# Kernel tuning notes

Measured on AMD Instinct MI355X. Metric: run time of the kernel, lower is better.

## Reference

```python
import jax, jax.numpy as jnp
import numpy as np

B, DIM, N = 16, 512, 4096


def setup_inputs() -> dict:
    key = jax.random.key(0)
    kx, kq, kk, kv = jax.random.split(key, 4)
    scale = 1.0 / np.sqrt(DIM)
    return {
        "x": jax.random.normal(kx, (B, DIM, N), dtype=jnp.float32),
        "Wq": jax.random.normal(kq, (DIM, DIM), dtype=jnp.float32) * scale,
        "Wk": jax.random.normal(kk, (DIM, DIM), dtype=jnp.float32) * scale,
        "Wv": jax.random.normal(kv, (DIM, DIM), dtype=jnp.float32) * scale,
    }


def reference(x, Wq, Wk, Wv):
    # x: [B, dim, N]; 1x1 conv over channel dim == matmul with [dim_out, dim_in]
    dim = x.shape[1]
    temperature = jnp.sqrt(jnp.asarray(dim, dtype=x.dtype))
    q = jnp.einsum("dc,bcn->bdn", Wq, x)  # [B, dim, N]
    k = jnp.einsum("dc,bcn->bdn", Wk, x)
    v = jnp.einsum("dc,bcn->bdn", Wv, x)
    # channel attention: contract over N points -> [B, dim, dim]
    attn = jnp.einsum("bdn,ben->bde", q / temperature, k)
    attn = jax.nn.softmax(attn, axis=-1)
    out = jnp.einsum("bde,ben->bdn", attn, v)  # [B, dim, N]
    return out
```

## Files before the change

kernel.cpp:

```cpp
#include <hip/hip_runtime.h>
#include <hip/hip_bf16.h>
#include <math.h>

#define DIMC 512
#define NPT  4096
#define BATCH 16
#define KSPLIT 4

typedef __bf16 bf16x4 __attribute__((ext_vector_type(4)));
typedef __bf16 bf16x8 __attribute__((ext_vector_type(8)));
typedef float  f32x4  __attribute__((ext_vector_type(4)));

typedef const __attribute__((address_space(1))) unsigned int guint;
typedef __attribute__((address_space(3))) unsigned int luint;

__device__ inline void gl_lds16(const void* g, void* l) {
  __builtin_amdgcn_global_load_lds((guint*)g, (luint*)l, 16, 0, 0);
}

__device__ inline unsigned short bfbits(float f) {
  union { __bf16 h; unsigned short u; } cv;
  cv.h = (__bf16)f;
  return cv.u;
}

__global__ __launch_bounds__(256, 4) void gram_split(
    const __bf16* __restrict__ xb, float* __restrict__ Gp)
{
  static const int TI[10] = {0,0,0,0,1,1,1,2,2,3};
  static const int TJ[10] = {0,1,2,3,1,2,3,2,3,3};
  const int id = blockIdx.x;
  const int xcd = id & 7, slot = id >> 3;
  const int g = slot / 10, t = slot % 10;
  const int pair = xcd + 8 * g;
  const int b = pair >> 2, s = pair & 3;
  const int m0 = TI[t] * 128, n0 = TJ[t] * 128;

  const __bf16* A = xb + (long)b * DIMC * NPT;
  float* C = Gp + (long)pair * DIMC * DIMC;

  __shared__ alignas(16) __bf16 As[128 * 32];
  __shared__ alignas(16) __bf16 Bs[128 * 32];

  const int tid  = threadIdx.x;
  const int wave = tid >> 6, lane = tid & 63;
  const int wr = wave >> 1, wc = wave & 1;
  const int q = lane >> 4, p = lane & 15;
  const int r4 = lane >> 2;
  const int koff = (lane & 3) * 8;

  f32x4 acc[4][4];
#pragma unroll
  for (int i = 0; i < 4; ++i)
#pragma unroll
    for (int j = 0; j < 4; ++j) acc[i][j] = (f32x4){0.f, 0.f, 0.f, 0.f};

  const __bf16* gA = A + (long)m0 * NPT;
  const __bf16* gB = A + (long)n0 * NPT;
  const int kbeg = s * (NPT / KSPLIT), kend = kbeg + NPT / KSPLIT;

  for (int k0 = kbeg; k0 < kend; k0 += 32) {
    __syncthreads();
#pragma unroll
    for (int h = 0; h < 2; ++h) {
      const int chunk = wave + h * 4;
      gl_lds16(gA + (long)(chunk * 16 + r4) * NPT + k0 + koff, &As[chunk * 512]);
      gl_lds16(gB + (long)(chunk * 16 + r4) * NPT + k0 + koff, &Bs[chunk * 512]);
    }
    __syncthreads();

    bf16x8 af[4], bfv[4];
#pragma unroll
    for (int i = 0; i < 4; ++i)
      af[i] = ((const bf16x8*)As)[(wr * 64 + i * 16 + p) * 4 + q];
#pragma unroll
    for (int j = 0; j < 4; ++j)
      bfv[j] = ((const bf16x8*)Bs)[(wc * 64 + j * 16 + p) * 4 + q];
#pragma unroll
    for (int i = 0; i < 4; ++i)
#pragma unroll
      for (int j = 0; j < 4; ++j)
        acc[i][j] = __builtin_amdgcn_mfma_f32_16x16x32_bf16(af[i], bfv[j], acc[i][j], 0, 0, 0);
  }

#pragma unroll
  for (int i = 0; i < 4; ++i) {
    const int row = m0 + wr * 64 + i * 16 + q * 4;
#pragma unroll
    for (int j = 0; j < 4; ++j) {
      const int col = n0 + wc * 64 + j * 16 + p;
#pragma unroll
      for (int r = 0; r < 4; ++r)
        C[(long)(row + r) * DIMC + col] = acc[i][j][r];
    }
  }
}

__global__ __launch_bounds__(256) void gram_reduce_mirror(
    const float* __restrict__ Gp, __bf16* __restrict__ Gh, __bf16* __restrict__ Gl)
{
  const int bid = blockIdx.x;
  const int b = bid / 36;
  int rem = bid % 36, I = 0;
  while (rem >= 8 - I) { rem -= 8 - I; ++I; }
  const int J = I + rem;

  __shared__ float T[64][65];
  const int tid = threadIdx.x;
  const int r = tid >> 2, c0 = (tid & 3) * 16;

  float v[16];
#pragma unroll
  for (int e = 0; e < 16; ++e) v[e] = 0.f;
#pragma unroll
  for (int s = 0; s < KSPLIT; ++s) {
    const float* src = Gp + (long)(b * KSPLIT + s) * DIMC * DIMC
                          + (long)(I * 64 + r) * DIMC + J * 64 + c0;
#pragma unroll
    for (int q = 0; q < 4; ++q) {
      float4 t4 = ((const float4*)src)[q];
      v[q * 4 + 0] += t4.x; v[q * 4 + 1] += t4.y;
      v[q * 4 + 2] += t4.z; v[q * 4 + 3] += t4.w;
    }
  }

  const long gbase = (long)b * DIMC * DIMC;
#pragma unroll
  for (int q = 0; q < 4; ++q) {
    bf16x4 h, l;
#pragma unroll
    for (int e = 0; e < 4; ++e) {
      float f = v[q * 4 + e];
      __bf16 hh = (__bf16)f;
      h[e] = hh; l[e] = (__bf16)(f - (float)hh);
    }
    const long o = gbase + (long)(I * 64 + r) * DIMC + J * 64 + c0 + q * 4;
    *(bf16x4*)(Gh + o) = h;
    *(bf16x4*)(Gl + o) = l;
  }
#pragma unroll
  for (int e = 0; e < 16; ++e) T[r][c0 + e] = v[e];
  __syncthreads();
  if (I != J) {
#pragma unroll
    for (int q = 0; q < 4; ++q) {
      bf16x4 h, l;
#pragma unroll
      for (int e = 0; e < 4; ++e) {
        float f = T[c0 + q * 4 + e][r];
        __bf16 hh = (__bf16)f;
        h[e] = hh; l[e] = (__bf16)(f - (float)hh);
      }
      const long o = gbase + (long)(J * 64 + r) * DIMC + I * 64 + c0 + q * 4;
      *(bf16x4*)(Gh + o) = h;
      *(bf16x4*)(Gl + o) = l;
    }
  }
}

template <bool SPLIT_OUT>
__global__ __launch_bounds__(256, 4) void gemm3_nt(
    const __bf16* __restrict__ Ah, const __bf16* __restrict__ Al,
    const __bf16* __restrict__ Bh, const __bf16* __restrict__ Bl,
    float* __restrict__ Cf, __bf16* __restrict__ Ch, __bf16* __restrict__ Cl,
    int K, long sA, long sB, long sC, float alpha)
{
  const int b = blockIdx.z;
  Ah += (long)b * sA;  Al += (long)b * sA;
  Bh += (long)b * sB;  Bl += (long)b * sB;
  const int m0 = blockIdx.y * 64, n0 = blockIdx.x * 128;

  __shared__ alignas(16) __bf16 sAh[64 * 32],  sAl[64 * 32];
  __shared__ alignas(16) __bf16 sBh[128 * 32], sBl[128 * 32];

  const int tid  = threadIdx.x;
  const int wave = tid >> 6, lane = tid & 63;
  const int wr = wave >> 1, wc = wave & 1;
  const int q = lane >> 4, p = lane & 15;
  const int r4 = lane >> 2;
  const int koff = (lane & 3) * 8;

  f32x4 acc[2][4];
#pragma unroll
  for (int i = 0; i < 2; ++i)
#pragma unroll
    for (int j = 0; j < 4; ++j) acc[i][j] = (f32x4){0.f, 0.f, 0.f, 0.f};

  const long arow = (long)(m0 + wave * 16 + r4) * K + koff;

  for (int k0 = 0; k0 < K; k0 += 32) {
    __syncthreads();
    gl_lds16(Ah + arow + k0, &sAh[wave * 512]);
    gl_lds16(Al + arow + k0, &sAl[wave * 512]);
#pragma unroll
    for (int h = 0; h < 2; ++h) {
      const int chunk = wave + h * 4;
      const long brow = (long)(n0 + chunk * 16 + r4) * K + koff + k0;
      gl_lds16(Bh + brow, &sBh[chunk * 512]);
      gl_lds16(Bl + brow, &sBl[chunk * 512]);
    }
    __syncthreads();

    bf16x8 fah[2], fal[2], fbh[4], fbl[4];
#pragma unroll
    for (int i = 0; i < 2; ++i) {
      const int idx = (wr * 32 + i * 16 + p) * 4 + q;
      fah[i] = ((const bf16x8*)sAh)[idx];
      fal[i] = ((const bf16x8*)sAl)[idx];
    }
#pragma unroll
    for (int j = 0; j < 4; ++j) {
      const int idx = (wc * 64 + j * 16 + p) * 4 + q;
      fbh[j] = ((const bf16x8*)sBh)[idx];
      fbl[j] = ((const bf16x8*)sBl)[idx];
    }
#pragma unroll
    for (int i = 0; i < 2; ++i)
#pragma unroll
      for (int j = 0; j < 4; ++j) {
        acc[i][j] = __builtin_amdgcn_mfma_f32_16x16x32_bf16(fah[i], fbh[j], acc[i][j], 0, 0, 0);
        acc[i][j] = __builtin_amdgcn_mfma_f32_16x16x32_bf16(fah[i], fbl[j], acc[i][j], 0, 0, 0);
        acc[i][j] = __builtin_amdgcn_mfma_f32_16x16x32_bf16(fal[i], fbh[j], acc[i][j], 0, 0, 0);
      }
  }

#pragma unroll
  for (int i = 0; i < 2; ++i) {
    const int row = m0 + wr * 32 + i * 16 + q * 4;
#pragma unroll
    for (int j = 0; j < 4; ++j) {
      const int col = n0 + wc * 64 + j * 16 + p;
#pragma unroll
      for (int r = 0; r < 4; ++r) {
        const float f = acc[i][j][r] * alpha;
        const long o = (long)b * sC + (long)(row + r) * DIMC + col;
        if (SPLIT_OUT) {
          __bf16 hh = (__bf16)f;
          Ch[o] = hh;
          Cl[o] = (__bf16)(f - (float)hh);
        } else {
          Cf[o] = f;
        }
      }
    }
  }
}

__global__ __launch_bounds__(256, 4) void gemm_nt64x128(
    const __bf16* __restrict__ A, const __bf16* __restrict__ B,
    __bf16* __restrict__ C, int K, long sA, long sB, long sC)
{
  const int b = blockIdx.z;
  A += (long)b * sA;  B += (long)b * sB;  C += (long)b * sC;
  const int m0 = blockIdx.y * 64, n0 = blockIdx.x * 128;

  __shared__ alignas(16) __bf16 As[64 * 32];
  __shared__ alignas(16) __bf16 Bs[128 * 32];

  const int tid  = threadIdx.x;
  const int wave = tid >> 6, lane = tid & 63;
  const int wr = wave >> 1, wc = wave & 1;
  const int q = lane >> 4, p = lane & 15;
  const int r4 = lane >> 2;
  const int koff = (lane & 3) * 8;

  f32x4 acc[2][4];
#pragma unroll
  for (int i = 0; i < 2; ++i)
#pragma unroll
    for (int j = 0; j < 4; ++j) acc[i][j] = (f32x4){0.f, 0.f, 0.f, 0.f};

  const long arow = (long)(m0 + wave * 16 + r4) * K + koff;

  for (int k0 = 0; k0 < K; k0 += 32) {
    __syncthreads();
    gl_lds16(A + arow + k0, &As[wave * 512]);
#pragma unroll
    for (int h = 0; h < 2; ++h) {
      const int chunk = wave + h * 4;
      gl_lds16(B + (long)(n0 + chunk * 16 + r4) * K + koff + k0, &Bs[chunk * 512]);
    }
    __syncthreads();

    bf16x8 af[2], bfv[4];
#pragma unroll
    for (int i = 0; i < 2; ++i)
      af[i] = ((const bf16x8*)As)[(wr * 32 + i * 16 + p) * 4 + q];
#pragma unroll
    for (int j = 0; j < 4; ++j)
      bfv[j] = ((const bf16x8*)Bs)[(wc * 64 + j * 16 + p) * 4 + q];
#pragma unroll
    for (int i = 0; i < 2; ++i)
#pragma unroll
      for (int j = 0; j < 4; ++j)
        acc[i][j] = __builtin_amdgcn_mfma_f32_16x16x32_bf16(af[i], bfv[j], acc[i][j], 0, 0, 0);
  }

#pragma unroll
  for (int i = 0; i < 2; ++i) {
    const int row = m0 + wr * 32 + i * 16 + q * 4;
#pragma unroll
    for (int j = 0; j < 4; ++j) {
      const int col = n0 + wc * 64 + j * 16 + p;
#pragma unroll
      for (int r = 0; r < 4; ++r)
        C[(long)(row + r) * DIMC + col] = (__bf16)acc[i][j][r];
    }
  }
}

__global__ __launch_bounds__(256, 2) void gemm_final(
    const __bf16* __restrict__ Mm, const __bf16* __restrict__ xt,
    float* __restrict__ out)
{
  const int id = blockIdx.x;
  const int xcd = id & 7, slot = id >> 3;
  const int g = slot >> 7, tile = slot & 127;
  const int b = xcd + 8 * g;
  const int m0 = (tile >> 5) * 128, n0 = (tile & 31) * 128;

  const __bf16* A = Mm + (long)b * DIMC * DIMC;
  const __bf16* B = xt + (long)b * NPT * DIMC;
  float* C = out + (long)b * DIMC * NPT;
  const int K = DIMC;

  __shared__ alignas(16) __bf16 As[128 * 32];
  __shared__ alignas(16) __bf16 Bs[128 * 32];

  const int tid  = threadIdx.x;
  const int wave = tid >> 6, lane = tid & 63;
  const int wr = wave >> 1, wc = wave & 1;
  const int q = lane >> 4, p = lane & 15;
  const int r4 = lane >> 2;
  const int koff = (lane & 3) * 8;

  f32x4 acc[4][4];
#pragma unroll
  for (int i = 0; i < 4; ++i)
#pragma unroll
    for (int j = 0; j < 4; ++j) acc[i][j] = (f32x4){0.f, 0.f, 0.f, 0.f};

  const __bf16* gA = A + (long)m0 * K;
  const __bf16* gB = B + (long)n0 * K;

  for (int k0 = 0; k0 < K; k0 += 32) {
    __syncthreads();
#pragma unroll
    for (int h = 0; h < 2; ++h) {
      const int chunk = wave + h * 4;
      gl_lds16(gA + (long)(chunk * 16 + r4) * K + k0 + koff, &As[chunk * 512]);
      gl_lds16(gB + (long)(chunk * 16 + r4) * K + k0 + koff, &Bs[chunk * 512]);
    }
    __syncthreads();

    bf16x8 af[4], bfv[4];
#pragma unroll
    for (int i = 0; i < 4; ++i)
      af[i] = ((const bf16x8*)As)[(wr * 64 + i * 16 + p) * 4 + q];
#pragma unroll
    for (int j = 0; j < 4; ++j)
      bfv[j] = ((const bf16x8*)Bs)[(wc * 64 + j * 16 + p) * 4 + q];
#pragma unroll
    for (int i = 0; i < 4; ++i)
#pragma unroll
      for (int j = 0; j < 4; ++j)
        acc[i][j] = __builtin_amdgcn_mfma_f32_16x16x32_bf16(af[i], bfv[j], acc[i][j], 0, 0, 0);
  }

#pragma unroll
  for (int i = 0; i < 4; ++i) {
    const int row = m0 + wr * 64 + i * 16 + q * 4;
#pragma unroll
    for (int j = 0; j < 4; ++j) {
      const int col = n0 + wc * 64 + j * 16 + p;
#pragma unroll
      for (int r = 0; r < 4; ++r)
        C[(long)(row + r) * NPT + col] = acc[i][j][r];
    }
  }
}

__global__ __launch_bounds__(256) void transpose_convert_x(
    const float* __restrict__ x, __bf16* __restrict__ xt,
    __bf16* __restrict__ xb)
{
  const int b = blockIdx.z;
  const int n0 = blockIdx.x * 64, c0 = blockIdx.y * 64;
  const float* X = x + (long)b * DIMC * NPT;
  __bf16* XT = xt + (long)b * NPT * DIMC;
  __bf16* XB = xb + (long)b * DIMC * NPT;

  __shared__ unsigned int D[64 * 34];

  const int t = threadIdx.x;
  const int tn = t & 15;
  const int tc = t >> 4;

#pragma unroll
  for (int pass = 0; pass < 2; ++pass) {
    const int c = pass * 32 + tc * 2;
    const float4 va = *(const float4*)(X + (long)(c0 + c) * NPT + n0 + tn * 4);
    const float4 vb = *(const float4*)(X + (long)(c0 + c + 1) * NPT + n0 + tn * 4);
    bf16x4 wa = {(__bf16)va.x, (__bf16)va.y, (__bf16)va.z, (__bf16)va.w};
    bf16x4 wb = {(__bf16)vb.x, (__bf16)vb.y, (__bf16)vb.z, (__bf16)vb.w};
    *(bf16x4*)(XB + (long)(c0 + c) * NPT + n0 + tn * 4) = wa;
    *(bf16x4*)(XB + (long)(c0 + c + 1) * NPT + n0 + tn * 4) = wb;
    const int cp = pass * 16 + tc;
    const float fa[4] = {va.x, va.y, va.z, va.w};
    const float fb[4] = {vb.x, vb.y, vb.z, vb.w};
#pragma unroll
    for (int i = 0; i < 4; ++i) {
      const unsigned int d = ((unsigned int)bfbits(fb[i]) << 16) | bfbits(fa[i]);
      D[(tn * 4 + i) * 34 + cp] = d;
    }
  }
  __syncthreads();

  const int n = t >> 2, ch = t & 3;
  const __bf16* Drow = (const __bf16*)&D[n * 34];
#pragma unroll
  for (int u = 0; u < 4; ++u) {
    const int unit = ch + u * 4;
    const uint2 w = *(const uint2*)(Drow + unit * 4);
    *(uint2*)(XT + (long)(n0 + n) * DIMC + c0 + unit * 4) = w;
  }
}

__global__ __launch_bounds__(256) void softmax_rows(
    const float* __restrict__ S, __bf16* __restrict__ P)
{
  const int row = blockIdx.x * 4 + (threadIdx.x >> 6);
  const int lane = threadIdx.x & 63;
  const float4* s4 = (const float4*)(S + (long)row * DIMC);
  float4 a = s4[lane * 2], b = s4[lane * 2 + 1];
  float v[8] = {a.x, a.y, a.z, a.w, b.x, b.y, b.z, b.w};
  float m = v[0];
#pragma unroll
  for (int i = 1; i < 8; ++i) m = fmaxf(m, v[i]);
#pragma unroll
  for (int off = 32; off > 0; off >>= 1) m = fmaxf(m, __shfl_xor(m, off));
  float e[8], sum = 0.f;
#pragma unroll
  for (int i = 0; i < 8; ++i) { e[i] = expf(v[i] - m); sum += e[i]; }
#pragma unroll
  for (int off = 32; off > 0; off >>= 1) sum += __shfl_xor(sum, off);
  const float inv = 1.0f / sum;
  bf16x8 o;
#pragma unroll
  for (int i = 0; i < 8; ++i) o[i] = (__bf16)(e[i] * inv);
  ((bf16x8*)(P + (long)row * DIMC))[lane] = o;
}

__global__ __launch_bounds__(256) void make_w(
    const float* __restrict__ Wq, const float* __restrict__ Wk,
    const float* __restrict__ Wv,
    __bf16* __restrict__ Wqh, __bf16* __restrict__ Wql,
    __bf16* __restrict__ Wkh, __bf16* __restrict__ Wkl,
    __bf16* __restrict__ WvT)
{
  const int i = blockIdx.x * 256 + threadIdx.x;
  float q = Wq[i];
  __bf16 qh = (__bf16)q; Wqh[i] = qh; Wql[i] = (__bf16)(q - (float)qh);
  float k = Wk[i];
  __bf16 kh = (__bf16)k; Wkh[i] = kh; Wkl[i] = (__bf16)(k - (float)kh);
  const int e = i >> 9, c = i & 511;
  WvT[(long)c * DIMC + e] = (__bf16)Wv[i];
}

extern "C" void kernel_launch(void* const* d_in, const int* in_sizes, int n_in,
                              void* d_out, int out_size, void* d_ws, size_t ws_size,
                              hipStream_t stream)
{
  const float* x  = (const float*)d_in[0];
  const float* Wq = (const float*)d_in[1];
  const float* Wk = (const float*)d_in[2];
  const float* Wv = (const float*)d_in[3];
  float* out = (float*)d_out;

  char* ws = (char*)d_ws;
  size_t off = 0;
  auto alloc = [&](size_t bytes) -> void* {
    void* p = ws + off;
    off += (bytes + 255) & ~(size_t)255;
    return p;
  };
  const long s2 = (long)DIMC * DIMC;

  __bf16* xt  = (__bf16*)alloc((size_t)BATCH * NPT * DIMC * 2);
  __bf16* xb  = (__bf16*)alloc((size_t)BATCH * DIMC * NPT * 2);
  float*  Gp  = (float*) alloc((size_t)KSPLIT * BATCH * s2 * 4);
  __bf16* Gh  = (__bf16*)alloc((size_t)BATCH * s2 * 2);
  __bf16* Gl  = (__bf16*)alloc((size_t)BATCH * s2 * 2);
  __bf16* Hh  = (__bf16*)alloc((size_t)BATCH * s2 * 2);
  __bf16* Hl  = (__bf16*)alloc((size_t)BATCH * s2 * 2);
  __bf16* Wqh = (__bf16*)alloc((size_t)s2 * 2);
  __bf16* Wql = (__bf16*)alloc((size_t)s2 * 2);
  __bf16* Wkh = (__bf16*)alloc((size_t)s2 * 2);
  __bf16* Wkl = (__bf16*)alloc((size_t)s2 * 2);
  __bf16* WvT = (__bf16*)alloc((size_t)s2 * 2);
  float*  S  = (float*)Gp;
  __bf16* P  = Gl;
  __bf16* Mm = Gh;

  make_w<<<DIMC * DIMC / 256, 256, 0, stream>>>(Wq, Wk, Wv, Wqh, Wql, Wkh, Wkl, WvT);
  transpose_convert_x<<<dim3(NPT / 64, DIMC / 64, BATCH), 256, 0, stream>>>(x, xt, xb);
  gram_split<<<640, 256, 0, stream>>>(xb, Gp);
  gram_reduce_mirror<<<BATCH * 36, 256, 0, stream>>>(Gp, Gh, Gl);
  gemm3_nt<true><<<dim3(4, 8, BATCH), 256, 0, stream>>>(
      Wqh, Wql, Gh, Gl, (float*)nullptr, Hh, Hl, DIMC, 0L, s2, s2, 1.0f);
  gemm3_nt<false><<<dim3(4, 8, BATCH), 256, 0, stream>>>(
      Hh, Hl, Wkh, Wkl, S, (__bf16*)nullptr, (__bf16*)nullptr,
      DIMC, s2, 0L, s2, 0.044194173824159216f);
  softmax_rows<<<BATCH * DIMC / 4, 256, 0, stream>>>(S, P);
  gemm_nt64x128<<<dim3(4, 8, BATCH), 256, 0, stream>>>(
      P, WvT, Mm, DIMC, s2, 0L, s2);
  gemm_final<<<2048, 256, 0, stream>>>(Mm, xt, out);
}
```

Baseline: 416.8 us.

## Drop transposed x copy; transpose B tile in registers inside final GEMM

Removes the transposed bf16 copy of x and replaces the transpose+convert kernel with a plain elementwise convert. The final GEMM now loads the channel-major xb tile through registers, repacks pairs of bf16 values and writes a padded transposed tile to shared memory. This saves writing and re-reading a full 64 MB intermediate. In exchange it loses the direct global-to-LDS async load for B and adds per-iteration VALU repacking.

```diff
diff --git a/kernel.cpp b/kernel.cpp
--- a/kernel.cpp
+++ b/kernel.cpp
@@ -16,12 +16,6 @@
 
 __device__ inline void gl_lds16(const void* g, void* l) {
   __builtin_amdgcn_global_load_lds((guint*)g, (luint*)l, 16, 0, 0);
-}
-
-__device__ inline unsigned short bfbits(float f) {
-  union { __bf16 h; unsigned short u; } cv;
-  cv.h = (__bf16)f;
-  return cv.u;
 }
 
 __global__ __launch_bounds__(256, 4) void gram_split(
@@ -310,7 +304,7 @@
 }
 
 __global__ __launch_bounds__(256, 2) void gemm_final(
-    const __bf16* __restrict__ Mm, const __bf16* __restrict__ xt,
+    const __bf16* __restrict__ Mm, const __bf16* __restrict__ xb,
     float* __restrict__ out)
 {
   const int id = blockIdx.x;
@@ -320,12 +314,12 @@
   const int m0 = (tile >> 5) * 128, n0 = (tile & 31) * 128;
 
   const __bf16* A = Mm + (long)b * DIMC * DIMC;
-  const __bf16* B = xt + (long)b * NPT * DIMC;
+  const __bf16* B = xb + (long)b * DIMC * NPT;
   float* C = out + (long)b * DIMC * NPT;
   const int K = DIMC;
 
   __shared__ alignas(16) __bf16 As[128 * 32];
-  __shared__ alignas(16) __bf16 Bs[128 * 32];
+  __shared__ alignas(16) unsigned int Bs[128 * 18];
 
   const int tid  = threadIdx.x;
   const int wave = tid >> 6, lane = tid & 63;
@@ -334,6 +328,9 @@
   const int r4 = lane >> 2;
   const int koff = (lane & 3) * 8;
 
+  const int ng = tid & 31;
+  const int cq = tid >> 5;
+
   f32x4 acc[4][4];
 #pragma unroll
   for (int i = 0; i < 4; ++i)
@@ -341,7 +338,6 @@
     for (int j = 0; j < 4; ++j) acc[i][j] = (f32x4){0.f, 0.f, 0.f, 0.f};
 
   const __bf16* gA = A + (long)m0 * K;
-  const __bf16* gB = B + (long)n0 * K;
 
   for (int k0 = 0; k0 < K; k0 += 32) {
     __syncthreads();
@@ -349,7 +345,27 @@
     for (int h = 0; h < 2; ++h) {
       const int chunk = wave + h * 4;
       gl_lds16(gA + (long)(chunk * 16 + r4) * K + k0 + koff, &As[chunk * 512]);
-      gl_lds16(gB + (long)(chunk * 16 + r4) * K + k0 + koff, &Bs[chunk * 512]);
+    }
+    uint2 rd[4];
+#pragma unroll
+    for (int r = 0; r < 4; ++r)
+      rd[r] = *(const uint2*)(B + (long)(k0 + cq * 4 + r) * NPT + n0 + ng * 4);
+#pragma unroll
+    for (int nn = 0; nn < 4; ++nn) {
+      const unsigned int s0 = (nn < 2) ? rd[0].x : rd[0].y;
+      const unsigned int s1 = (nn < 2) ? rd[1].x : rd[1].y;
+      const unsigned int s2 = (nn < 2) ? rd[2].x : rd[2].y;
+      const unsigned int s3 = (nn < 2) ? rd[3].x : rd[3].y;
+      unsigned int o01, o23;
+      if (nn & 1) {
+        o01 = (s0 >> 16) | (s1 & 0xffff0000u);
+        o23 = (s2 >> 16) | (s3 & 0xffff0000u);
+      } else {
+        o01 = (s0 & 0xffffu) | (s1 << 16);
+        o23 = (s2 & 0xffffu) | (s3 << 16);
+      }
+      uint2 o; o.x = o01; o.y = o23;
+      *(uint2*)&Bs[(ng * 4 + nn) * 18 + cq * 2] = o;
     }
     __syncthreads();
 
@@ -358,8 +374,14 @@
     for (int i = 0; i < 4; ++i)
       af[i] = ((const bf16x8*)As)[(wr * 64 + i * 16 + p) * 4 + q];
 #pragma unroll
-    for (int j = 0; j < 4; ++j)
-      bfv[j] = ((const bf16x8*)Bs)[(wc * 64 + j * 16 + p) * 4 + q];
+    for (int j = 0; j < 4; ++j) {
+      const unsigned int* bp = &Bs[(wc * 64 + j * 16 + p) * 18 + q * 4];
+      const uint2 lo = *(const uint2*)bp;
+      const uint2 hi = *(const uint2*)(bp + 2);
+      union { uint4 u; bf16x8 v; } cvt;
+      cvt.u.x = lo.x; cvt.u.y = lo.y; cvt.u.z = hi.x; cvt.u.w = hi.y;
+      bfv[j] = cvt.v;
+    }
 #pragma unroll
     for (int i = 0; i < 4; ++i)
 #pragma unroll
@@ -380,49 +402,20 @@
   }
 }
 
-__global__ __launch_bounds__(256) void transpose_convert_x(
-    const float* __restrict__ x, __bf16* __restrict__ xt,
-    __bf16* __restrict__ xb)
-{
-  const int b = blockIdx.z;
-  const int n0 = blockIdx.x * 64, c0 = blockIdx.y * 64;
-  const float* X = x + (long)b * DIMC * NPT;
-  __bf16* XT = xt + (long)b * NPT * DIMC;
-  __bf16* XB = xb + (long)b * DIMC * NPT;
-
-  __shared__ unsigned int D[64 * 34];
-
-  const int t = threadIdx.x;
-  const int tn = t & 15;
-  const int tc = t >> 4;
-
-#pragma unroll
-  for (int pass = 0; pass < 2; ++pass) {
-    const int c = pass * 32 + tc * 2;
-    const float4 va = *(const float4*)(X + (long)(c0 + c) * NPT + n0 + tn * 4);
-    const float4 vb = *(const float4*)(X + (long)(c0 + c + 1) * NPT + n0 + tn * 4);
-    bf16x4 wa = {(__bf16)va.x, (__bf16)va.y, (__bf16)va.z, (__bf16)va.w};
-    bf16x4 wb = {(__bf16)vb.x, (__bf16)vb.y, (__bf16)vb.z, (__bf16)vb.w};
-    *(bf16x4*)(XB + (long)(c0 + c) * NPT + n0 + tn * 4) = wa;
-    *(bf16x4*)(XB + (long)(c0 + c + 1) * NPT + n0 + tn * 4) = wb;
-    const int cp = pass * 16 + tc;
-    const float fa[4] = {va.x, va.y, va.z, va.w};
-    const float fb[4] = {vb.x, vb.y, vb.z, vb.w};
-#pragma unroll
-    for (int i = 0; i < 4; ++i) {
-      const unsigned int d = ((unsigned int)bfbits(fb[i]) << 16) | bfbits(fa[i]);
-      D[(tn * 4 + i) * 34 + cp] = d;
-    }
-  }
-  __syncthreads();
-
-  const int n = t >> 2, ch = t & 3;
-  const __bf16* Drow = (const __bf16*)&D[n * 34];
-#pragma unroll
-  for (int u = 0; u < 4; ++u) {
-    const int unit = ch + u * 4;
-    const uint2 w = *(const uint2*)(Drow + unit * 4);
-    *(uint2*)(XT + (long)(n0 + n) * DIMC + c0 + unit * 4) = w;
+__global__ __launch_bounds__(256) void convert_x(
+    const float* __restrict__ x, __bf16* __restrict__ xb)
+{
+  const long total8 = (long)BATCH * DIMC * NPT / 8;
+  const long stride = (long)gridDim.x * 256;
+  for (long i = blockIdx.x * 256 + threadIdx.x; i < total8; i += stride) {
+    const f32x4 a = ((const f32x4*)x)[2 * i];
+    const f32x4 b = ((const f32x4*)x)[2 * i + 1];
+    bf16x8 o;
+    o[0] = (__bf16)a[0]; o[1] = (__bf16)a[1];
+    o[2] = (__bf16)a[2]; o[3] = (__bf16)a[3];
+    o[4] = (__bf16)b[0]; o[5] = (__bf16)b[1];
+    o[6] = (__bf16)b[2]; o[7] = (__bf16)b[3];
+    ((bf16x8*)xb)[i] = o;
   }
 }
 
@@ -486,7 +479,6 @@
   };
   const long s2 = (long)DIMC * DIMC;
 
-  __bf16* xt  = (__bf16*)alloc((size_t)BATCH * NPT * DIMC * 2);
   __bf16* xb  = (__bf16*)alloc((size_t)BATCH * DIMC * NPT * 2);
   float*  Gp  = (float*) alloc((size_t)KSPLIT * BATCH * s2 * 4);
   __bf16* Gh  = (__bf16*)alloc((size_t)BATCH * s2 * 2);
@@ -503,7 +495,7 @@
   __bf16* Mm = Gh;
 
   make_w<<<DIMC * DIMC / 256, 256, 0, stream>>>(Wq, Wk, Wv, Wqh, Wql, Wkh, Wkl, WvT);
-  transpose_convert_x<<<dim3(NPT / 64, DIMC / 64, BATCH), 256, 0, stream>>>(x, xt, xb);
+  convert_x<<<2048, 256, 0, stream>>>(x, xb);
   gram_split<<<640, 256, 0, stream>>>(xb, Gp);
   gram_reduce_mirror<<<BATCH * 36, 256, 0, stream>>>(Gp, Gh, Gl);
   gemm3_nt<true><<<dim3(4, 8, BATCH), 256, 0, stream>>>(
@@ -514,5 +506,5 @@
   softmax_rows<<<BATCH * DIMC / 4, 256, 0, stream>>>(S, P);
   gemm_nt64x128<<<dim3(4, 8, BATCH), 256, 0, stream>>>(
       P, WvT, Mm, DIMC, s2, 0L, s2);
-  gemm_final<<<2048, 256, 0, stream>>>(Mm, xt, out);
-}
+  gemm_final<<<2048, 256, 0, stream>>>(Mm, xb, out);
+}
```

Result: faster. 394.3 us (-5.4%).
